# Performance work log

Hardware: AMD Instinct MI355X
Metric: run time of the kernel (lower is better)

The kernel has to match this reference:

```python
import jax, jax.numpy as jnp
import numpy as np

DIM = 64
PATCH = 8
KH = KW = 7
K = KH * KW
PAD = 3


def conv2d(x, w, pad):
    return jax.lax.conv_general_dilated(
        x, w, window_strides=(1, 1), padding=[(pad, pad), (pad, pad)],
        dimension_numbers=('NCHW', 'OIHW', 'NCHW'))


def deform_conv2d(x, offset, mask, weight):
    # torchvision modulated deformable conv v2, stride=1, dilation=1, pad=PAD
    B, C, H, W = x.shape
    off = offset.reshape(B, K, 2, H, W)  # channel pairs are (dy, dx)
    ky, kx = jnp.meshgrid(jnp.arange(KH), jnp.arange(KW), indexing='ij')
    ky = ky.reshape(K).astype(x.dtype)
    kx = kx.reshape(K).astype(x.dtype)
    hh = jnp.arange(H, dtype=x.dtype)
    ww = jnp.arange(W, dtype=x.dtype)
    # sampling locations: p0 - pad + p_k + offset, shape [B,K,H,W]
    y = hh[None, None, :, None] - PAD + ky[None, :, None, None] + off[:, :, 0]
    xx = ww[None, None, None, :] - PAD + kx[None, :, None, None] + off[:, :, 1]

    y0 = jnp.floor(y)
    x0 = jnp.floor(xx)
    wy = y - y0
    wx = xx - x0

    img_flat = x.reshape(B, C, H * W)

    def gather(yi, xi):
        valid = (yi >= 0) & (yi < H) & (xi >= 0) & (xi < W)
        yc = jnp.clip(yi, 0, H - 1).astype(jnp.int32)
        xc = jnp.clip(xi, 0, W - 1).astype(jnp.int32)
        lin = (yc * W + xc).reshape(B, -1)  # [B, K*H*W]
        v = jax.vmap(lambda im, idx: im[:, idx])(img_flat, lin)  # [B,C,K*H*W]
        v = v.reshape(B, C, K, H, W)
        return v * valid[:, None].astype(x.dtype)

    val = ((1 - wy) * (1 - wx))[:, None] * gather(y0, x0) \
        + ((1 - wy) * wx)[:, None] * gather(y0, x0 + 1) \
        + (wy * (1 - wx))[:, None] * gather(y0 + 1, x0) \
        + (wy * wx)[:, None] * gather(y0 + 1, x0 + 1)
    val = val * mask[:, None]  # modulation, [B,C,K,H,W]
    wf = weight.reshape(weight.shape[0], weight.shape[1], K)
    return jnp.einsum('bckhw,ock->bohw', val, wf)


def setup_inputs() -> dict:
    key = jax.random.key(0)
    ks = jax.random.split(key, 12)
    B, C, H, W = 1, DIM, 192, 192
    s = 0.05
    return {
        'enc': jax.random.normal(ks[0], (B, C, H, W), jnp.float32),
        'dec': jax.random.normal(ks[1], (B, C, H, W), jnp.float32),
        'inverse_offset': jax.random.normal(ks[2], (B, 2 * K, H, W), jnp.float32),
        'inverse_weight': jax.random.uniform(ks[3], (B, K, H, W), jnp.float32),
        'w_proj_in': jax.random.normal(ks[4], (C, C, 1, 1), jnp.float32) * s,
        'fft_w': 1.0 + 0.1 * jax.random.normal(ks[5], (C, 1, 1, PATCH, PATCH // 2 + 1), jnp.float32),
        'w_proj_out': jax.random.normal(ks[6], (2 * C, 2 * C, 1, 1), jnp.float32) * s,
        'w_deform': jax.random.normal(ks[7], (C, C, KH, KW), jnp.float32) * s,
        'w_conv1': jax.random.normal(ks[8], (C, C, 1, 1), jnp.float32) * s,
        'w_conv2': jax.random.normal(ks[9], (C, C, 3, 3), jnp.float32) * s,
    }


def reference(enc, dec, inverse_offset, inverse_weight, w_proj_in, fft_w,
              w_proj_out, w_deform, w_conv1, w_conv2):
    B, C, h, w = enc.shape
    reverse = deform_conv2d(enc, inverse_offset, inverse_weight, w_deform)
    reverse = conv2d(reverse, w_conv1, 0)

    e = conv2d(enc, w_proj_in, 0)
    # check_image_size: pad H,W to multiples of PATCH (no-op for 192)
    ph = (-h) % PATCH
    pw = (-w) % PATCH
    e = jnp.pad(e, ((0, 0), (0, 0), (0, ph), (0, pw)))
    Hp, Wp = h + ph, w + pw
    # [B,C,h',w',p1,p2]
    xp = e.reshape(B, C, Hp // PATCH, PATCH, Wp // PATCH, PATCH).transpose(0, 1, 2, 4, 3, 5)
    xf = jnp.fft.rfft2(xp.astype(jnp.float32)) * fft_w  # fft_w [C,1,1,8,5] broadcasts
    xp = jnp.fft.irfft2(xf, s=(PATCH, PATCH))
    e = xp.transpose(0, 1, 2, 4, 3, 5).reshape(B, C, Hp, Wp)[:, :, :h, :w]

    e = e + reverse
    e = conv2d(e, w_conv2, 1)
    feat = jnp.concatenate([e, dec], axis=1)
    feat = conv2d(feat, w_proj_out, 0)
    x1, x2 = jnp.split(feat, 2, axis=1)  # SimpleGate
    return x1 * x2
```

## Files before the change

kernel.cpp:

```cpp
#include <hip/hip_runtime.h>
#include <math.h>

#define CH    64
#define WW    192
#define HH    192
#define HWSZ  (192*192)
#define KK    49
#define ROWP  68
#define SROW  72
#define C3ROW 72
#define OROW  136

typedef __attribute__((ext_vector_type(8))) short s16x8;
typedef __attribute__((ext_vector_type(4))) float f32x4;

__device__ __forceinline__ unsigned short f2bf(float f) {
    union { float f; unsigned u; } v; v.f = f;
    unsigned u = v.u + 0x7FFFu + ((v.u >> 16) & 1u);
    return (unsigned short)(u >> 16);
}

__device__ __forceinline__ unsigned pkbf(float lo, float hi) {
    return __builtin_amdgcn_perm(__float_as_uint(hi) + 0x8000u,
                                 __float_as_uint(lo) + 0x8000u, 0x07060302u);
}

__device__ const float c_cos8[8] = {
    1.f, 0.70710678118654752f, 0.f, -0.70710678118654752f,
   -1.f, -0.70710678118654752f, 0.f, 0.70710678118654752f };

__global__ __launch_bounds__(256) void k_prep(
    const float* __restrict__ fw,
    const float* __restrict__ wd,
    const float* __restrict__ w2,
    const float* __restrict__ wc1,
    const float* __restrict__ wpo,
    const float* __restrict__ wpi,
    float* __restrict__ krT,
    short* __restrict__ wA,
    short* __restrict__ w2A,
    short* __restrict__ wpoA,
    short* __restrict__ wpiA)
{
    int tid = blockIdx.x * blockDim.x + threadIdx.x;
    int nt  = gridDim.x * blockDim.x;
    for (int t = tid; t < 64 * 64; t += nt) {
        int uv = t >> 6, c = t & 63;
        int u = uv >> 3, v = uv & 7;
        float acc = 0.f;
        for (int ky = 0; ky < 8; ky++)
            for (int kx = 0; kx < 8; kx++) {
                float wv = (kx <= 4) ? fw[c * 40 + ky * 5 + kx]
                                     : fw[c * 40 + ((8 - ky) & 7) * 5 + (8 - kx)];
                acc += wv * c_cos8[(ky * u + kx * v) & 7];
            }
        krT[uv * 64 + c] = acc * (1.f / 64.f);
    }
    for (int t = tid; t < 9 * 4096; t += nt) {
        int tap = t / 4096, rem = t & 4095;
        int o = rem >> 6, c = rem & 63;
        float v = w2[(o * 64 + c) * 9 + tap];
        int fi = tap * 8 + (o >> 4) * 2 + (c >> 5);
        int ln = ((c >> 3) & 3) * 16 + (o & 15);
        w2A[fi * 512 + ln * 8 + (c & 7)] = (short)f2bf(v);
    }
    for (int t = tid; t < 128 * 128; t += nt) {
        int o = t >> 7, c = t & 127;
        int fi = (o >> 4) * 4 + (c >> 5);
        int ln = ((c >> 3) & 3) * 16 + (o & 15);
        wpoA[fi * 512 + ln * 8 + (c & 7)] = (short)f2bf(wpo[t]);
    }
    for (int t = tid; t < 64 * 64; t += nt) {
        int o = t >> 6, c = t & 63;
        int fi = (o >> 4) * 2 + (c >> 5);
        int ln = ((c >> 3) & 3) * 16 + (o & 15);
        wpiA[fi * 512 + ln * 8 + (c & 7)] = (short)f2bf(wpi[t]);
    }

    __shared__ float wdk [64 * ROWP];
    __shared__ float wc1s[64 * ROWP];
    int k = blockIdx.x;
    int t = threadIdx.x;
#pragma unroll
    for (int r = 0; r < 16; r++) {
        int idx = t + r * 256;
        int o = idx >> 6, c = idx & 63;
        wdk [o * ROWP + c] = wd[(o * 64 + c) * KK + k];
        wc1s[o * ROWP + c] = wc1[o * 64 + c];
    }
    __syncthreads();

    int ot = (t >> 4) * 4, cb = (t & 15) * 4;
    float a[4][4];
#pragma unroll
    for (int i = 0; i < 4; i++)
#pragma unroll
        for (int j = 0; j < 4; j++) a[i][j] = 0.f;
    for (int o = 0; o < 64; o++) {
        float wv_[4], sv_[4];
#pragma unroll
        for (int i = 0; i < 4; i++) wv_[i] = wc1s[(ot + i) * ROWP + o];
#pragma unroll
        for (int j = 0; j < 4; j++) sv_[j] = wdk[o * ROWP + cb + j];
#pragma unroll
        for (int i = 0; i < 4; i++)
#pragma unroll
            for (int j = 0; j < 4; j++) a[i][j] += wv_[i] * sv_[j];
    }
#pragma unroll
    for (int i = 0; i < 4; i++)
#pragma unroll
        for (int j = 0; j < 4; j++) {
            int o2 = ot + i, c = cb + j;
            int tt = o2 >> 4, m = o2 & 15;
            int kt = c >> 5, q = (c >> 3) & 3, jj = c & 7;
            int ln = q * 16 + m;
            wA[(k * 8 + tt * 2 + kt) * 512 + ln * 8 + jj] = (short)f2bf(a[i][j]);
        }
}

__global__ __launch_bounds__(256) void k_trans(
    const float* __restrict__ enc, unsigned short* __restrict__ encH)
{
    __shared__ float s[64 * 65];
    int t = threadIdx.x;
    int base = blockIdx.x * 64;
#pragma unroll
    for (int r = 0; r < 16; r++) {
        int idx = t + r * 256;
        int p = idx & 63, c = idx >> 6;
        s[p * 65 + c] = enc[c * HWSZ + base + p];
    }
    __syncthreads();
#pragma unroll
    for (int r = 0; r < 8; r++) {
        int idx = t + r * 256;
        int pr = idx & 31, p = idx >> 5;
        ((unsigned*)encH)[(base + p) * 32 + pr] =
            pkbf(s[p * 65 + 2 * pr], s[p * 65 + 2 * pr + 1]);
    }
}

#define REDW 20

__global__ __launch_bounds__(256) void k_deform(
    const unsigned short* __restrict__ encH, const float* __restrict__ off,
    const float* __restrict__ msk, const short* __restrict__ wA,
    float* __restrict__ rev)
{
    __shared__ __align__(16) short sm[4][16 * SROW];
    __shared__ __align__(16) float red[2 * 64 * REDW];

    int t = threadIdx.x;
    int lane = t & 63, w = t >> 6;
    int b = blockIdx.x;
    int xcd = b & 7, blk = b >> 3;
    int gy  = xcd * 24 + blk / 12;
    int gx0 = (blk % 12) * 16;

    int sp = lane >> 2, g = lane & 3;
    int sgx  = gx0 + sp;
    int gp_s = gy * WW + sgx;
    int n = lane & 15, q = lane >> 4;
    short* smw = &sm[w][0];

    f32x4 acc[4];
#pragma unroll
    for (int ot = 0; ot < 4; ot++) acc[ot] = (f32x4){0.f, 0.f, 0.f, 0.f};

    int kstart = (w == 0) ? 0 : 13 + (w - 1) * 12;
    int kend   = (w == 0) ? 13 : kstart + 12;

    float dy = off[(2 * kstart) * HWSZ + gp_s];
    float dx = off[(2 * kstart + 1) * HWSZ + gp_s];
    float mm = msk[kstart * HWSZ + gp_s];

#pragma unroll 1
    for (int k = kstart; k < kend; k++) {
        int ky = k / 7, kx = k % 7;
        float y = (float)(gy  - 3 + ky) + dy;
        float x = (float)(sgx - 3 + kx) + dx;
        float y0f = floorf(y), x0f = floorf(x);
        float wy = y - y0f, wx = x - x0f;
        int iy0 = (int)y0f, ix0 = (int)x0f;
        int iy1 = iy0 + 1, ix1 = ix0 + 1;
        bool vy0 = (iy0 >= 0) & (iy0 < HH);
        bool vy1 = (iy1 >= 0) & (iy1 < HH);
        bool vx0 = (ix0 >= 0) & (ix0 < WW);
        bool vx1 = (ix1 >= 0) & (ix1 < WW);
        int iy0c = min(max(iy0, 0), HH - 1), iy1c = min(max(iy1, 0), HH - 1);
        int ix0c = min(max(ix0, 0), WW - 1), ix1c = min(max(ix1, 0), WW - 1);
        float a00 = (vy0 & vx0) ? (1.f - wy) * (1.f - wx) * mm : 0.f;
        float a01 = (vy0 & vx1) ? (1.f - wy) * wx * mm : 0.f;
        float a10 = (vy1 & vx0) ? wy * (1.f - wx) * mm : 0.f;
        float a11 = (vy1 & vx1) ? wy * wx * mm : 0.f;

        const unsigned short* b00p = encH + (iy0c * WW + ix0c) * 64 + g * 16;
        const unsigned short* b01p = encH + (iy0c * WW + ix1c) * 64 + g * 16;
        const unsigned short* b10p = encH + (iy1c * WW + ix0c) * 64 + g * 16;
        const unsigned short* b11p = encH + (iy1c * WW + ix1c) * 64 + g * 16;
        uint4 u00[2], u01[2], u10[2], u11[2];
        u00[0] = *(const uint4*)b00p;  u00[1] = *(const uint4*)(b00p + 8);
        u01[0] = *(const uint4*)b01p;  u01[1] = *(const uint4*)(b01p + 8);
        u10[0] = *(const uint4*)b10p;  u10[1] = *(const uint4*)(b10p + 8);
        u11[0] = *(const uint4*)b11p;  u11[1] = *(const uint4*)(b11p + 8);

        float dyn = 0.f, dxn = 0.f, mmn = 0.f;
        if (k + 1 < kend) {
            dyn = off[(2 * k + 2) * HWSZ + gp_s];
            dxn = off[(2 * k + 3) * HWSZ + gp_s];
            mmn = msk[(k + 1) * HWSZ + gp_s];
        }

        s16x8 af[8];
#pragma unroll
        for (int f = 0; f < 8; f++)
            af[f] = *(const s16x8*)&wA[(k * 8 + f) * 512 + lane * 8];

        float res[16];
#pragma unroll
        for (int j = 0; j < 16; j++) res[j] = 0.f;
        {
            const uint4* cs[4] = {u00, u01, u10, u11};
            float       aw[4] = {a00, a01, a10, a11};
#pragma unroll
            for (int cix = 0; cix < 4; cix++) {
                unsigned uu[8] = {cs[cix][0].x, cs[cix][0].y, cs[cix][0].z, cs[cix][0].w,
                                  cs[cix][1].x, cs[cix][1].y, cs[cix][1].z, cs[cix][1].w};
                float a = aw[cix];
#pragma unroll
                for (int j = 0; j < 8; j++) {
                    res[2 * j]     += a * __uint_as_float(uu[j] << 16);
                    res[2 * j + 1] += a * __uint_as_float(uu[j] & 0xffff0000u);
                }
            }
        }
        unsigned pk[8];
#pragma unroll
        for (int j = 0; j < 8; j++) pk[j] = pkbf(res[2 * j], res[2 * j + 1]);
        *(uint4*)&smw[sp * SROW + g * 16]     = make_uint4(pk[0], pk[1], pk[2], pk[3]);
        *(uint4*)&smw[sp * SROW + g * 16 + 8] = make_uint4(pk[4], pk[5], pk[6], pk[7]);

        s16x8 b0 = *(const s16x8*)&smw[n * SROW +  0 + q * 8];
        s16x8 b1 = *(const s16x8*)&smw[n * SROW + 32 + q * 8];

#pragma unroll
        for (int ot = 0; ot < 4; ot++) {
            acc[ot] = __builtin_amdgcn_mfma_f32_16x16x32_bf16(af[ot * 2],     b0, acc[ot], 0, 0, 0);
            acc[ot] = __builtin_amdgcn_mfma_f32_16x16x32_bf16(af[ot * 2 + 1], b1, acc[ot], 0, 0, 0);
        }

        dy = dyn; dx = dxn; mm = mmn;
    }

    if (w >= 2) {
        float* rp = &red[((w - 2) * 64 + lane) * REDW];
#pragma unroll
        for (int ot = 0; ot < 4; ot++)
            *(float4*)&rp[ot * 4] = make_float4(acc[ot][0], acc[ot][1], acc[ot][2], acc[ot][3]);
    }
    __syncthreads();
    if (w < 2) {
        const float* rp = &red[(w * 64 + lane) * REDW];
#pragma unroll
        for (int ot = 0; ot < 4; ot++) {
            float4 v = *(const float4*)&rp[ot * 4];
            acc[ot][0] += v.x; acc[ot][1] += v.y;
            acc[ot][2] += v.z; acc[ot][3] += v.w;
        }
    }
    __syncthreads();
    if (w == 1) {
        float* rp = &red[lane * REDW];
#pragma unroll
        for (int ot = 0; ot < 4; ot++)
            *(float4*)&rp[ot * 4] = make_float4(acc[ot][0], acc[ot][1], acc[ot][2], acc[ot][3]);
    }
    __syncthreads();
    if (w == 0) {
        const float* rp = &red[lane * REDW];
#pragma unroll
        for (int ot = 0; ot < 4; ot++) {
            float4 v = *(const float4*)&rp[ot * 4];
            acc[ot][0] += v.x; acc[ot][1] += v.y;
            acc[ot][2] += v.z; acc[ot][3] += v.w;
        }
        int gp_m = gy * WW + gx0 + n;
#pragma unroll
        for (int ot = 0; ot < 4; ot++) {
            float4 rv = make_float4(acc[ot][0], acc[ot][1], acc[ot][2], acc[ot][3]);
            *(float4*)&rev[gp_m * 64 + ot * 16 + q * 4] = rv;
        }
    }
}

__global__ __launch_bounds__(256) void k_fft(
    const unsigned short* __restrict__ encH, const short* __restrict__ wpiA,
    const float* __restrict__ krT, float* __restrict__ e1)
{
    __shared__ __align__(16) short sbf[64 * SROW];
    __shared__ __align__(16) float e0[64 * ROWP];
    int t = threadIdx.x;
    int pbx = blockIdx.x % 24, pby = blockIdx.x / 24;
    int gx0 = pbx * 8, gy0 = pby * 8;

#pragma unroll
    for (int r = 0; r < 2; r++) {
        int idx = t + r * 256;
        int px = idx >> 3, g8 = idx & 7;
        int gy = gy0 + (px >> 3), gx = gx0 + (px & 7);
        *(uint4*)&sbf[px * SROW + g8 * 8] =
            *(const uint4*)&encH[(gy * WW + gx) * 64 + g8 * 8];
    }
    __syncthreads();

    int lane = t & 63, w = t >> 6;
    int n = lane & 15, q = lane >> 4;
    s16x8 a0 = *(const s16x8*)&wpiA[(w * 2 + 0) * 512 + lane * 8];
    s16x8 a1 = *(const s16x8*)&wpiA[(w * 2 + 1) * 512 + lane * 8];
#pragma unroll
    for (int j = 0; j < 4; j++) {
        s16x8 b0 = *(const s16x8*)&sbf[(j * 16 + n) * SROW +  0 + q * 8];
        s16x8 b1 = *(const s16x8*)&sbf[(j * 16 + n) * SROW + 32 + q * 8];
        f32x4 acc = {0.f, 0.f, 0.f, 0.f};
        acc = __builtin_amdgcn_mfma_f32_16x16x32_bf16(a0, b0, acc, 0, 0, 0);
        acc = __builtin_amdgcn_mfma_f32_16x16x32_bf16(a1, b1, acc, 0, 0, 0);
#pragma unroll
        for (int r = 0; r < 4; r++)
            e0[(j * 16 + n) * ROWP + w * 16 + q * 4 + r] = acc[r];
    }
    __syncthreads();

    int o = t & 63;
    int yb = t >> 6;
#pragma unroll
    for (int yy = 0; yy < 2; yy++) {
        int y = yb + yy * 4;
        float outr[8];
#pragma unroll
        for (int x = 0; x < 8; x++) outr[x] = 0.f;
#pragma unroll
        for (int u = 0; u < 8; u++) {
            int ry = (y - u + 8) & 7;
            float row[8];
#pragma unroll
            for (int rx = 0; rx < 8; rx++)
                row[rx] = e0[(ry * 8 + rx) * ROWP + o];
#pragma unroll
            for (int v = 0; v < 8; v++) {
                float kv = krT[(u * 8 + v) * 64 + o];
#pragma unroll
                for (int x = 0; x < 8; x++)
                    outr[x] += kv * row[(x - v + 8) & 7];
            }
        }
        int gy = gy0 + y;
#pragma unroll
        for (int x = 0; x < 8; x++)
            e1[(gy * WW + gx0 + x) * 64 + o] = outr[x];
    }
}

__global__ __launch_bounds__(256) void k_c3out(
    const float* __restrict__ e1, const float* __restrict__ rev,
    const short* __restrict__ w2A, const float* __restrict__ dec,
    const short* __restrict__ wpoA, float* __restrict__ out)
{
    __shared__ __align__(16) short sm[4][54 * C3ROW];
    int t = threadIdx.x;
    int lane = t & 63, w = t >> 6;
    int b = blockIdx.x;
    int xcd = b & 7, blk = b >> 3;
    int gy  = xcd * 24 + blk / 3;
    int gx0 = (blk % 3) * 64 + w * 16;
    short* smw = &sm[w][0];
    int n = lane & 15, q = lane >> 4;

    for (int r = 0; r < 14; r++) {
        int u = lane + r * 64;
        if (u < 864) {
            int rp = u >> 4, g = u & 15;
            int row = rp / 18, pxl = rp - row * 18;
            int gyy = gy + row - 1, gxx = gx0 + pxl - 1;
            float4 v = make_float4(0.f, 0.f, 0.f, 0.f);
            if (gyy >= 0 && gyy < HH && gxx >= 0 && gxx < WW) {
                int gp = (gyy * WW + gxx) * 64 + g * 4;
                float4 va = *(const float4*)&e1[gp];
                float4 vb = *(const float4*)&rev[gp];
                v.x = va.x + vb.x; v.y = va.y + vb.y;
                v.z = va.z + vb.z; v.w = va.w + vb.w;
            }
            *(uint2*)&smw[rp * C3ROW + g * 4] = make_uint2(pkbf(v.x, v.y), pkbf(v.z, v.w));
        }
    }

    f32x4 acc[4];
#pragma unroll
    for (int ot = 0; ot < 4; ot++) acc[ot] = (f32x4){0.f, 0.f, 0.f, 0.f};

#pragma unroll 1
    for (int tap = 0; tap < 9; tap++) {
        int dy = tap / 3, dx = tap - dy * 3;
        int rp = dy * 18 + n + dx;
        s16x8 b0 = *(const s16x8*)&smw[rp * C3ROW +  0 + q * 8];
        s16x8 b1 = *(const s16x8*)&smw[rp * C3ROW + 32 + q * 8];
#pragma unroll
        for (int ot = 0; ot < 4; ot++) {
            s16x8 a0 = *(const s16x8*)&w2A[(tap * 8 + ot * 2 + 0) * 512 + lane * 8];
            s16x8 a1 = *(const s16x8*)&w2A[(tap * 8 + ot * 2 + 1) * 512 + lane * 8];
            acc[ot] = __builtin_amdgcn_mfma_f32_16x16x32_bf16(a0, b0, acc[ot], 0, 0, 0);
            acc[ot] = __builtin_amdgcn_mfma_f32_16x16x32_bf16(a1, b1, acc[ot], 0, 0, 0);
        }
    }

#pragma unroll
    for (int ot = 0; ot < 4; ot++) {
        unsigned lo = pkbf(acc[ot][0], acc[ot][1]);
        unsigned hi = pkbf(acc[ot][2], acc[ot][3]);
        *(uint2*)&smw[n * OROW + ot * 16 + q * 4] = make_uint2(lo, hi);
    }
    {
        int gp = gy * WW + gx0 + n;
        unsigned pk[8];
#pragma unroll
        for (int i = 0; i < 8; i++) {
            float va = dec[(q * 16 + 2 * i)     * HWSZ + gp];
            float vb = dec[(q * 16 + 2 * i + 1) * HWSZ + gp];
            pk[i] = pkbf(va, vb);
        }
        *(uint4*)&smw[n * OROW + 64 + q * 16]     = make_uint4(pk[0], pk[1], pk[2], pk[3]);
        *(uint4*)&smw[n * OROW + 64 + q * 16 + 8] = make_uint4(pk[4], pk[5], pk[6], pk[7]);
    }

    f32x4 go[8];
#pragma unroll
    for (int ot = 0; ot < 8; ot++) go[ot] = (f32x4){0.f, 0.f, 0.f, 0.f};

#pragma unroll 1
    for (int kt = 0; kt < 4; kt++) {
        s16x8 bb = *(const s16x8*)&smw[n * OROW + kt * 32 + q * 8];
#pragma unroll
        for (int ot = 0; ot < 8; ot++) {
            s16x8 aa = *(const s16x8*)&wpoA[(ot * 4 + kt) * 512 + lane * 8];
            go[ot] = __builtin_amdgcn_mfma_f32_16x16x32_bf16(aa, bb, go[ot], 0, 0, 0);
        }
    }

    int gp = gy * WW + gx0 + n;
#pragma unroll
    for (int ot = 0; ot < 4; ot++)
#pragma unroll
        for (int r = 0; r < 4; r++)
            out[(ot * 16 + q * 4 + r) * HWSZ + gp] = go[ot][r] * go[ot + 4][r];
}

extern "C" void kernel_launch(void* const* d_in, const int* in_sizes, int n_in,
                              void* d_out, int out_size, void* d_ws, size_t ws_size,
                              hipStream_t stream)
{
    const float* enc  = (const float*)d_in[0];
    const float* dec  = (const float*)d_in[1];
    const float* ioff = (const float*)d_in[2];
    const float* iwt  = (const float*)d_in[3];
    const float* wpi  = (const float*)d_in[4];
    const float* fw   = (const float*)d_in[5];
    const float* wpo  = (const float*)d_in[6];
    const float* wd   = (const float*)d_in[7];
    const float* wc1  = (const float*)d_in[8];
    const float* wc2  = (const float*)d_in[9];
    float* out = (float*)d_out;
    float* ws  = (float*)d_ws;

    float*          krT  = ws;
    float*          rev  = ws + 4096;
    float*          e1   = ws + 2363392;
    unsigned short* encH = (unsigned short*)(ws + 4722688);
    short*          wA   = (short*)(ws + 5902336);
    short*          w2A  = (short*)(ws + 6002688);
    short*          wpoA = (short*)(ws + 6021120);
    short*          wpiA = (short*)(ws + 6029312);

    hipLaunchKernelGGL(k_prep,   dim3(49),   dim3(256), 0, stream,
                       fw, wd, wc2, wc1, wpo, wpi, krT, wA, w2A, wpoA, wpiA);
    hipLaunchKernelGGL(k_trans,  dim3(576),  dim3(256), 0, stream, enc, encH);
    hipLaunchKernelGGL(k_deform, dim3(2304), dim3(256), 0, stream, encH, ioff, iwt, wA, rev);
    hipLaunchKernelGGL(k_fft,    dim3(576),  dim3(256), 0, stream, encH, wpiA, krT, e1);
    hipLaunchKernelGGL(k_c3out,  dim3(576),  dim3(256), 0, stream, e1, rev, w2A, dec, wpoA, out);
}
```

Before: 215.0 us.

## Apply bilinear weights after MFMA and feed corner samples directly as operands

Drops the per-lane bilinear interpolation, bf16 repacking and LDS round-trip in the deformable conv. The four corner pixels are now loaded straight from global memory in the MFMA B-operand layout, and each goes through its own MFMA chain. The per-pixel corner weights are then applied to the fp32 partial results before accumulating. This removes LDS traffic and the unpack/pack VALU work, but it needs four times as many MFMAs per kernel tap plus extra FMAs to combine the partials. The kernel-tap index math is also replaced by incremental counters.

```diff
diff --git a/kernel.cpp b/kernel.cpp
--- a/kernel.cpp
+++ b/kernel.cpp
@@ -148,7 +148,6 @@
     const float* __restrict__ msk, const short* __restrict__ wA,
     float* __restrict__ rev)
 {
-    __shared__ __align__(16) short sm[4][16 * SROW];
     __shared__ __align__(16) float red[2 * 64 * REDW];
 
     int t = threadIdx.x;
@@ -158,15 +157,14 @@
     int gy  = xcd * 24 + blk / 12;
     int gx0 = (blk % 12) * 16;
 
-    int sp = lane >> 2, g = lane & 3;
-    int sgx  = gx0 + sp;
+    int n = lane & 15, q = lane >> 4;
+    int sgx  = gx0 + n;
     int gp_s = gy * WW + sgx;
-    int n = lane & 15, q = lane >> 4;
-    short* smw = &sm[w][0];
 
     f32x4 acc[4];
 #pragma unroll
     for (int ot = 0; ot < 4; ot++) acc[ot] = (f32x4){0.f, 0.f, 0.f, 0.f};
+    const f32x4 zf = (f32x4){0.f, 0.f, 0.f, 0.f};
 
     int kstart = (w == 0) ? 0 : 13 + (w - 1) * 12;
     int kend   = (w == 0) ? 13 : kstart + 12;
@@ -175,9 +173,10 @@
     float dx = off[(2 * kstart + 1) * HWSZ + gp_s];
     float mm = msk[kstart * HWSZ + gp_s];
 
+    int ky = kstart / 7, kx = kstart % 7;
+
 #pragma unroll 1
     for (int k = kstart; k < kend; k++) {
-        int ky = k / 7, kx = k % 7;
         float y = (float)(gy  - 3 + ky) + dy;
         float x = (float)(sgx - 3 + kx) + dx;
         float y0f = floorf(y), x0f = floorf(x);
@@ -195,15 +194,15 @@
         float a10 = (vy1 & vx0) ? wy * (1.f - wx) * mm : 0.f;
         float a11 = (vy1 & vx1) ? wy * wx * mm : 0.f;
 
-        const unsigned short* b00p = encH + (iy0c * WW + ix0c) * 64 + g * 16;
-        const unsigned short* b01p = encH + (iy0c * WW + ix1c) * 64 + g * 16;
-        const unsigned short* b10p = encH + (iy1c * WW + ix0c) * 64 + g * 16;
-        const unsigned short* b11p = encH + (iy1c * WW + ix1c) * 64 + g * 16;
-        uint4 u00[2], u01[2], u10[2], u11[2];
-        u00[0] = *(const uint4*)b00p;  u00[1] = *(const uint4*)(b00p + 8);
-        u01[0] = *(const uint4*)b01p;  u01[1] = *(const uint4*)(b01p + 8);
-        u10[0] = *(const uint4*)b10p;  u10[1] = *(const uint4*)(b10p + 8);
-        u11[0] = *(const uint4*)b11p;  u11[1] = *(const uint4*)(b11p + 8);
+        int r0 = iy0c * WW, r1 = iy1c * WW;
+        const unsigned short* p00 = encH + ((r0 + ix0c) << 6) + (q << 3);
+        const unsigned short* p01 = encH + ((r0 + ix1c) << 6) + (q << 3);
+        const unsigned short* p10 = encH + ((r1 + ix0c) << 6) + (q << 3);
+        const unsigned short* p11 = encH + ((r1 + ix1c) << 6) + (q << 3);
+        s16x8 b00a = *(const s16x8*)p00, b00b = *(const s16x8*)(p00 + 32);
+        s16x8 b01a = *(const s16x8*)p01, b01b = *(const s16x8*)(p01 + 32);
+        s16x8 b10a = *(const s16x8*)p10, b10b = *(const s16x8*)(p10 + 32);
+        s16x8 b11a = *(const s16x8*)p11, b11b = *(const s16x8*)(p11 + 32);
 
         float dyn = 0.f, dxn = 0.f, mmn = 0.f;
         if (k + 1 < kend) {
@@ -212,45 +211,26 @@
             mmn = msk[(k + 1) * HWSZ + gp_s];
         }
 
-        s16x8 af[8];
-#pragma unroll
-        for (int f = 0; f < 8; f++)
-            af[f] = *(const s16x8*)&wA[(k * 8 + f) * 512 + lane * 8];
-
-        float res[16];
-#pragma unroll
-        for (int j = 0; j < 16; j++) res[j] = 0.f;
-        {
-            const uint4* cs[4] = {u00, u01, u10, u11};
-            float       aw[4] = {a00, a01, a10, a11};
-#pragma unroll
-            for (int cix = 0; cix < 4; cix++) {
-                unsigned uu[8] = {cs[cix][0].x, cs[cix][0].y, cs[cix][0].z, cs[cix][0].w,
-                                  cs[cix][1].x, cs[cix][1].y, cs[cix][1].z, cs[cix][1].w};
-                float a = aw[cix];
-#pragma unroll
-                for (int j = 0; j < 8; j++) {
-                    res[2 * j]     += a * __uint_as_float(uu[j] << 16);
-                    res[2 * j + 1] += a * __uint_as_float(uu[j] & 0xffff0000u);
-                }
-            }
-        }
-        unsigned pk[8];
-#pragma unroll
-        for (int j = 0; j < 8; j++) pk[j] = pkbf(res[2 * j], res[2 * j + 1]);
-        *(uint4*)&smw[sp * SROW + g * 16]     = make_uint4(pk[0], pk[1], pk[2], pk[3]);
-        *(uint4*)&smw[sp * SROW + g * 16 + 8] = make_uint4(pk[4], pk[5], pk[6], pk[7]);
-
-        s16x8 b0 = *(const s16x8*)&smw[n * SROW +  0 + q * 8];
-        s16x8 b1 = *(const s16x8*)&smw[n * SROW + 32 + q * 8];
-
 #pragma unroll
         for (int ot = 0; ot < 4; ot++) {
-            acc[ot] = __builtin_amdgcn_mfma_f32_16x16x32_bf16(af[ot * 2],     b0, acc[ot], 0, 0, 0);
-            acc[ot] = __builtin_amdgcn_mfma_f32_16x16x32_bf16(af[ot * 2 + 1], b1, acc[ot], 0, 0, 0);
+            s16x8 af0 = *(const s16x8*)&wA[(k * 8 + ot * 2 + 0) * 512 + lane * 8];
+            s16x8 af1 = *(const s16x8*)&wA[(k * 8 + ot * 2 + 1) * 512 + lane * 8];
+            f32x4 t00 = __builtin_amdgcn_mfma_f32_16x16x32_bf16(af0, b00a, zf, 0, 0, 0);
+            t00       = __builtin_amdgcn_mfma_f32_16x16x32_bf16(af1, b00b, t00, 0, 0, 0);
+            f32x4 t01 = __builtin_amdgcn_mfma_f32_16x16x32_bf16(af0, b01a, zf, 0, 0, 0);
+            t01       = __builtin_amdgcn_mfma_f32_16x16x32_bf16(af1, b01b, t01, 0, 0, 0);
+            f32x4 t10 = __builtin_amdgcn_mfma_f32_16x16x32_bf16(af0, b10a, zf, 0, 0, 0);
+            t10       = __builtin_amdgcn_mfma_f32_16x16x32_bf16(af1, b10b, t10, 0, 0, 0);
+            f32x4 t11 = __builtin_amdgcn_mfma_f32_16x16x32_bf16(af0, b11a, zf, 0, 0, 0);
+            t11       = __builtin_amdgcn_mfma_f32_16x16x32_bf16(af1, b11b, t11, 0, 0, 0);
+#pragma unroll
+            for (int r = 0; r < 4; r++)
+                acc[ot][r] += a00 * t00[r] + a01 * t01[r]
+                            + a10 * t10[r] + a11 * t11[r];
         }
 
         dy = dyn; dx = dxn; mm = mmn;
+        kx++; if (kx == 7) { kx = 0; ky++; }
     }
 
     if (w >= 2) {
```

Result: slower. 284.6 us (+32.3%).
